# Performance work log

Hardware: AMD Instinct MI355X
Metric: run time of the kernel (lower is better)

## Reference

```python
import jax, jax.numpy as jnp
import numpy as np

EMBED_DIM = 1024
NUM_HEADS = 16
HEAD_DIM = EMBED_DIM // NUM_HEADS
SCALE = HEAD_DIM ** -0.5


def setup_inputs() -> dict:
    key = jax.random.key(0)
    k_x, k_qkv, k_proj = jax.random.split(key, 3)
    x = jax.random.normal(k_x, (2, 2048, EMBED_DIM), dtype=jnp.float32)
    # nn.Linear weights: [out_features, in_features]
    w_qkv = jax.random.normal(k_qkv, (3 * EMBED_DIM, EMBED_DIM), dtype=jnp.float32) * (EMBED_DIM ** -0.5)
    w_proj = jax.random.normal(k_proj, (EMBED_DIM, EMBED_DIM), dtype=jnp.float32) * (EMBED_DIM ** -0.5)
    return {"x": x, "w_qkv": w_qkv, "w_proj": w_proj}


def reference(x, w_qkv, w_proj):
    B, N, C = x.shape
    # fused QKV projection: [B,N,3C]
    qkv = jnp.einsum('bnc,oc->bno', x, w_qkv)
    qkv = qkv.reshape(B, N, 3, NUM_HEADS, HEAD_DIM)
    q, k, v = jnp.moveaxis(qkv, 2, 0)  # each [B, N, H, D]
    q = q.transpose(0, 2, 1, 3)  # [B, H, N, D]
    k = k.transpose(0, 2, 1, 3)
    v = v.transpose(0, 2, 1, 3)
    # scaled dot-product attention (eval mode: dropout_p=0, non-causal)
    scores = jnp.einsum('bhqd,bhkd->bhqk', q, k) * SCALE
    attn = jax.nn.softmax(scores, axis=-1)
    out = jnp.einsum('bhqk,bhkd->bhqd', attn, v)  # [B, H, N, D]
    out = out.transpose(0, 2, 1, 3).reshape(B, N, C)
    return jnp.einsum('bnc,oc->bno', out, w_proj)
```

## Files before the change

### kernel.cpp

```cpp
#include <hip/hip_runtime.h>
#include <hip/hip_bf16.h>

typedef __bf16 bf16;
typedef __bf16 bf16x8 __attribute__((ext_vector_type(8)));
typedef __bf16 bf16x4 __attribute__((ext_vector_type(4)));
typedef float f32x4 __attribute__((ext_vector_type(4)));

#define MFMA16(a, b, c) __builtin_amdgcn_mfma_f32_16x16x32_bf16(a, b, c, 0, 0, 0)

__global__ void cvt_kernel(const float* __restrict__ in, bf16* __restrict__ out, int n4) {
    int i = blockIdx.x * blockDim.x + threadIdx.x;
    if (i < n4) {
        float4 f = ((const float4*)in)[i];
        bf16x4 o;
        o[0] = (bf16)f.x; o[1] = (bf16)f.y; o[2] = (bf16)f.z; o[3] = (bf16)f.w;
        ((bf16x4*)out)[i] = o;
    }
}

__global__ __launch_bounds__(256, 2) void gemm_qkv(
    const bf16* __restrict__ A, const bf16* __restrict__ Bm,
    bf16* __restrict__ qo, bf16* __restrict__ ko, bf16* __restrict__ vo)
{
    const int K = 1024;
    __shared__ bf16 As[128][40];
    __shared__ bf16 Bs[128][40];
    const int tid = threadIdx.x;
    const int wave = tid >> 6, lane = tid & 63;
    const int lrow = lane & 15, quad = lane >> 4;
    const int wm = (wave >> 1) * 64, wn = (wave & 1) * 64;
    const int si = tid >> 2, sk = (tid & 3) * 8;

    const bf16* Ap = A + (long)(blockIdx.x * 128 + si) * K + sk;
    const bf16* Bp = Bm + (long)(blockIdx.y * 128 + si) * K + sk;

    f32x4 acc[4][4] = {};

    for (int k0 = 0; k0 < K; k0 += 32) {
        bf16x8 a0 = *(const bf16x8*)(Ap + k0);
        bf16x8 a1 = *(const bf16x8*)(Ap + (long)64 * K + k0);
        bf16x8 b0 = *(const bf16x8*)(Bp + k0);
        bf16x8 b1 = *(const bf16x8*)(Bp + (long)64 * K + k0);
        __syncthreads();
        *(bf16x8*)&As[si][sk]      = a0;
        *(bf16x8*)&As[si + 64][sk] = a1;
        *(bf16x8*)&Bs[si][sk]      = b0;
        *(bf16x8*)&Bs[si + 64][sk] = b1;
        __syncthreads();
        bf16x8 af[4], bfr[4];
#pragma unroll
        for (int i = 0; i < 4; i++) af[i] = *(const bf16x8*)&As[wm + i * 16 + lrow][quad * 8];
#pragma unroll
        for (int j = 0; j < 4; j++) bfr[j] = *(const bf16x8*)&Bs[wn + j * 16 + lrow][quad * 8];
#pragma unroll
        for (int i = 0; i < 4; i++)
#pragma unroll
            for (int j = 0; j < 4; j++)
                acc[i][j] = MFMA16(af[i], bfr[j], acc[i][j]);
    }

    const int gm0 = blockIdx.x * 128 + wm;
    const int go0 = blockIdx.y * 128 + wn;

    if (blockIdx.y < 16) {
        const bool isQ = blockIdx.y < 8;
        bf16* dst = isQ ? qo : ko;
        const float sc = isQ ? 0.125f : 1.0f;
#pragma unroll
        for (int i = 0; i < 4; i++) {
#pragma unroll
            for (int r = 0; r < 4; r++) {
                int gm = gm0 + i * 16 + quad * 4 + r;
                int b = gm >> 11, n = gm & 2047;
#pragma unroll
                for (int j = 0; j < 4; j++) {
                    int o = go0 + j * 16 + lrow;
                    int rem = o & 1023;
                    int h = rem >> 6, d = rem & 63;
                    long idx = (((long)(b * 16 + h)) * 2048 + n) * 64 + d;
                    dst[idx] = (bf16)(acc[i][j][r] * sc);
                }
            }
        }
    } else {
#pragma unroll
        for (int i = 0; i < 4; i++) {
            int gmb = gm0 + i * 16 + quad * 4;
            int b = gmb >> 11, nb = gmb & 2047;
#pragma unroll
            for (int j = 0; j < 4; j++) {
                int o = go0 + j * 16 + lrow;
                int rem = o & 1023;
                int h = rem >> 6, d = rem & 63;
                bf16x4 pk;
#pragma unroll
                for (int r = 0; r < 4; r++) pk[r] = (bf16)acc[i][j][r];
                *(bf16x4*)&vo[(((long)(b * 16 + h)) * 64 + d) * 2048 + nb] = pk;
            }
        }
    }
}

__global__ __launch_bounds__(256, 2) void attn_kernel(
    const bf16* __restrict__ q, const bf16* __restrict__ k,
    const bf16* __restrict__ vt, bf16* __restrict__ o)
{
    __shared__ bf16 Ks[64][72];
    __shared__ bf16 Vts[64][72];
    __shared__ bf16 QP[128][72];

    const int tid = threadIdx.x, wave = tid >> 6, lane = tid & 63;
    const int lrow = lane & 15, quad = lane >> 4;
    const int bh = blockIdx.x, qt = blockIdx.y;
    const bf16* Qp = q + ((long)bh * 2048 + qt * 128) * 64;
    const bf16* Kp = k + (long)bh * 2048 * 64;
    const bf16* Vp = vt + (long)bh * 64 * 2048;

    {
        int r0 = tid >> 3, g = (tid & 7) * 8;
#pragma unroll
        for (int p = 0; p < 4; p++)
            *(bf16x8*)&QP[r0 + p * 32][g] = *(const bf16x8*)&Qp[(r0 + p * 32) * 64 + g];
    }
    __syncthreads();
    bf16x8 qf[2][2];
#pragma unroll
    for (int t = 0; t < 2; t++)
#pragma unroll
        for (int ks = 0; ks < 2; ks++)
            qf[t][ks] = *(const bf16x8*)&QP[wave * 32 + t * 16 + lrow][ks * 32 + quad * 8];

    bf16(*Ps)[72] = (bf16(*)[72])QP + wave * 32;

    float mst[2] = {-1e30f, -1e30f}, lst[2] = {0.0f, 0.0f};
    f32x4 oacc[2][4] = {};

    for (int kv = 0; kv < 32; kv++) {
        const int r0 = tid >> 3, g = (tid & 7) * 8;
        const bf16* Kt = Kp + kv * 64 * 64;
        bf16x8 k0v = *(const bf16x8*)&Kt[r0 * 64 + g];
        bf16x8 k1v = *(const bf16x8*)&Kt[(r0 + 32) * 64 + g];
        bf16x8 v0v = *(const bf16x8*)&Vp[(long)r0 * 2048 + kv * 64 + g];
        bf16x8 v1v = *(const bf16x8*)&Vp[(long)(r0 + 32) * 2048 + kv * 64 + g];
        __syncthreads();
        *(bf16x8*)&Ks[r0][g]       = k0v;
        *(bf16x8*)&Ks[r0 + 32][g]  = k1v;
        *(bf16x8*)&Vts[r0][g]      = v0v;
        *(bf16x8*)&Vts[r0 + 32][g] = v1v;
        __syncthreads();

        f32x4 sacc[2][4] = {};
#pragma unroll
        for (int ks = 0; ks < 2; ks++) {
            bf16x8 kf[4];
#pragma unroll
            for (int n = 0; n < 4; n++) kf[n] = *(const bf16x8*)&Ks[n * 16 + lrow][ks * 32 + quad * 8];
#pragma unroll
            for (int t = 0; t < 2; t++)
#pragma unroll
                for (int n = 0; n < 4; n++)
                    sacc[t][n] = MFMA16(kf[n], qf[t][ks], sacc[t][n]);
        }

#pragma unroll
        for (int t = 0; t < 2; t++) {
            float mx = -1e30f;
#pragma unroll
            for (int n = 0; n < 4; n++)
#pragma unroll
                for (int r = 0; r < 4; r++) mx = fmaxf(mx, sacc[t][n][r]);
            mx = fmaxf(mx, __shfl_xor(mx, 16, 64));
            mx = fmaxf(mx, __shfl_xor(mx, 32, 64));
            float mnew = fmaxf(mst[t], mx);
            float alpha = __expf(mst[t] - mnew);
            mst[t] = mnew;
            float rsum = 0.0f;
#pragma unroll
            for (int n = 0; n < 4; n++) {
                bf16x4 pk;
#pragma unroll
                for (int r = 0; r < 4; r++) {
                    float p = __expf(sacc[t][n][r] - mnew);
                    rsum += p;
                    pk[r] = (bf16)p;
                }
                *(bf16x4*)&Ps[t * 16 + lrow][n * 16 + quad * 4] = pk;
            }
            rsum += __shfl_xor(rsum, 16, 64);
            rsum += __shfl_xor(rsum, 32, 64);
            lst[t] = lst[t] * alpha + rsum;
            float a0 = __shfl(alpha, quad * 4 + 0, 64);
            float a1 = __shfl(alpha, quad * 4 + 1, 64);
            float a2 = __shfl(alpha, quad * 4 + 2, 64);
            float a3 = __shfl(alpha, quad * 4 + 3, 64);
#pragma unroll
            for (int jd = 0; jd < 4; jd++) {
                oacc[t][jd][0] *= a0; oacc[t][jd][1] *= a1;
                oacc[t][jd][2] *= a2; oacc[t][jd][3] *= a3;
            }
        }

#pragma unroll
        for (int c = 0; c < 2; c++) {
            bf16x8 vf[4];
#pragma unroll
            for (int jd = 0; jd < 4; jd++)
                vf[jd] = *(const bf16x8*)&Vts[jd * 16 + lrow][c * 32 + quad * 8];
#pragma unroll
            for (int t = 0; t < 2; t++) {
                bf16x8 pf = *(const bf16x8*)&Ps[t * 16 + lrow][c * 32 + quad * 8];
#pragma unroll
                for (int jd = 0; jd < 4; jd++)
                    oacc[t][jd] = MFMA16(pf, vf[jd], oacc[t][jd]);
            }
        }
    }

    const int b = bh >> 4, h = bh & 15;
#pragma unroll
    for (int t = 0; t < 2; t++) {
        float linv = 1.0f / lst[t];
#pragma unroll
        for (int r = 0; r < 4; r++) {
            float lr = __shfl(linv, quad * 4 + r, 64);
            int n = qt * 128 + wave * 32 + t * 16 + quad * 4 + r;
#pragma unroll
            for (int jd = 0; jd < 4; jd++)
                o[((long)(b * 2048 + n)) * 1024 + h * 64 + jd * 16 + lrow] = (bf16)(oacc[t][jd][r] * lr);
        }
    }
}

__global__ __launch_bounds__(256, 2) void gemm_proj(
    const bf16* __restrict__ A, const bf16* __restrict__ Bm, float* __restrict__ out)
{
    const int K = 1024;
    __shared__ bf16 As[128][40];
    __shared__ bf16 Bs[128][40];
    const int tid = threadIdx.x;
    const int wave = tid >> 6, lane = tid & 63;
    const int lrow = lane & 15, quad = lane >> 4;
    const int wm = (wave >> 1) * 64, wn = (wave & 1) * 64;
    const int si = tid >> 2, sk = (tid & 3) * 8;

    const bf16* Ap = A + (long)(blockIdx.x * 128 + si) * K + sk;
    const bf16* Bp = Bm + (long)(blockIdx.y * 128 + si) * K + sk;

    f32x4 acc[4][4] = {};

    for (int k0 = 0; k0 < K; k0 += 32) {
        bf16x8 a0 = *(const bf16x8*)(Ap + k0);
        bf16x8 a1 = *(const bf16x8*)(Ap + (long)64 * K + k0);
        bf16x8 b0 = *(const bf16x8*)(Bp + k0);
        bf16x8 b1 = *(const bf16x8*)(Bp + (long)64 * K + k0);
        __syncthreads();
        *(bf16x8*)&As[si][sk]      = a0;
        *(bf16x8*)&As[si + 64][sk] = a1;
        *(bf16x8*)&Bs[si][sk]      = b0;
        *(bf16x8*)&Bs[si + 64][sk] = b1;
        __syncthreads();
        bf16x8 af[4], bfr[4];
#pragma unroll
        for (int i = 0; i < 4; i++) af[i] = *(const bf16x8*)&As[wm + i * 16 + lrow][quad * 8];
#pragma unroll
        for (int j = 0; j < 4; j++) bfr[j] = *(const bf16x8*)&Bs[wn + j * 16 + lrow][quad * 8];
#pragma unroll
        for (int i = 0; i < 4; i++)
#pragma unroll
            for (int j = 0; j < 4; j++)
                acc[i][j] = MFMA16(af[i], bfr[j], acc[i][j]);
    }

    const int gm0 = blockIdx.x * 128 + wm;
    const int go0 = blockIdx.y * 128 + wn;
#pragma unroll
    for (int i = 0; i < 4; i++)
#pragma unroll
        for (int r = 0; r < 4; r++) {
            int gm = gm0 + i * 16 + quad * 4 + r;
#pragma unroll
            for (int j = 0; j < 4; j++) {
                int o = go0 + j * 16 + lrow;
                out[(long)gm * 1024 + o] = acc[i][j][r];
            }
        }
}

extern "C" void kernel_launch(void* const* d_in, const int* in_sizes, int n_in,
                              void* d_out, int out_size, void* d_ws, size_t ws_size,
                              hipStream_t stream) {
    const float* x      = (const float*)d_in[0];
    const float* w_qkv  = (const float*)d_in[1];
    const float* w_proj = (const float*)d_in[2];
    float* out = (float*)d_out;

    bf16* ws = (bf16*)d_ws;
    bf16* xb     = ws;
    bf16* wqkvb  = xb + 4096 * 1024;
    bf16* wprojb = wqkvb + 3072 * 1024;
    bf16* qb     = wprojb + 1024 * 1024;
    bf16* kb     = qb + 2 * 16 * 2048 * 64;
    bf16* vb     = kb + 2 * 16 * 2048 * 64;
    bf16* ob     = vb + 2 * 16 * 2048 * 64;

    cvt_kernel<<<(4096 * 1024 / 4 + 255) / 256, 256, 0, stream>>>(x, xb, 4096 * 1024 / 4);
    cvt_kernel<<<(3072 * 1024 / 4 + 255) / 256, 256, 0, stream>>>(w_qkv, wqkvb, 3072 * 1024 / 4);
    cvt_kernel<<<(1024 * 1024 / 4 + 255) / 256, 256, 0, stream>>>(w_proj, wprojb, 1024 * 1024 / 4);

    gemm_qkv<<<dim3(32, 24), 256, 0, stream>>>(xb, wqkvb, qb, kb, vb);
    attn_kernel<<<dim3(32, 16), 256, 0, stream>>>(qb, kb, vb, ob);
    gemm_proj<<<dim3(32, 8), 256, 0, stream>>>(ob, wprojb, out);
}
```

Baseline: 205.3 us.

## Use direct global-to-LDS loads in GEMMs, register-direct K/V in attention

Both GEMMs now stage tiles with global_load_lds (direct global-to-LDS DMA) into unpadded 32-wide tiles, so the register round-trip disappears. The cost is more LDS bank conflicts on the fragment reads. The attention kernel drops shared-memory staging of Q, K and V: each wave loads its fragments straight from global memory into registers, prefetches the next K tile, and keeps only a per-wave P buffer, which removes the block-wide barriers. Attention grid indexing is flattened so heads vary fastest, and the projection GEMM uses 128x64 tiles to launch twice as many blocks. The trade-off is redundant global/L2 traffic for K/V across waves and uncoalesced strided V loads.

```diff
diff --git a/kernel.cpp b/kernel.cpp
--- a/kernel.cpp
+++ b/kernel.cpp
@@ -7,6 +7,12 @@
 typedef float f32x4 __attribute__((ext_vector_type(4)));
 
 #define MFMA16(a, b, c) __builtin_amdgcn_mfma_f32_16x16x32_bf16(a, b, c, 0, 0, 0)
+
+__device__ __forceinline__ void gll(const bf16* g, bf16* l) {
+    __builtin_amdgcn_global_load_lds(
+        (const __attribute__((address_space(1))) unsigned int*)g,
+        (__attribute__((address_space(3))) unsigned int*)l, 16, 0, 0);
+}
 
 __global__ void cvt_kernel(const float* __restrict__ in, bf16* __restrict__ out, int n4) {
     int i = blockIdx.x * blockDim.x + threadIdx.x;
@@ -22,36 +28,31 @@
     const bf16* __restrict__ A, const bf16* __restrict__ Bm,
     bf16* __restrict__ qo, bf16* __restrict__ ko, bf16* __restrict__ vo)
 {
-    const int K = 1024;
-    __shared__ bf16 As[128][40];
-    __shared__ bf16 Bs[128][40];
+    __shared__ bf16 As[128 * 32];
+    __shared__ bf16 Bs[128 * 32];
     const int tid = threadIdx.x;
     const int wave = tid >> 6, lane = tid & 63;
     const int lrow = lane & 15, quad = lane >> 4;
     const int wm = (wave >> 1) * 64, wn = (wave & 1) * 64;
-    const int si = tid >> 2, sk = (tid & 3) * 8;
-
-    const bf16* Ap = A + (long)(blockIdx.x * 128 + si) * K + sk;
-    const bf16* Bp = Bm + (long)(blockIdx.y * 128 + si) * K + sk;
+    const int row = tid >> 2, kcol = (tid & 3) * 8;
+
+    const bf16* Ap = A + (long)(blockIdx.x * 128 + row) * 1024 + kcol;
+    const bf16* Bp = Bm + (long)(blockIdx.y * 128 + row) * 1024 + kcol;
 
     f32x4 acc[4][4] = {};
 
-    for (int k0 = 0; k0 < K; k0 += 32) {
-        bf16x8 a0 = *(const bf16x8*)(Ap + k0);
-        bf16x8 a1 = *(const bf16x8*)(Ap + (long)64 * K + k0);
-        bf16x8 b0 = *(const bf16x8*)(Bp + k0);
-        bf16x8 b1 = *(const bf16x8*)(Bp + (long)64 * K + k0);
+    for (int k0 = 0; k0 < 1024; k0 += 32) {
         __syncthreads();
-        *(bf16x8*)&As[si][sk]      = a0;
-        *(bf16x8*)&As[si + 64][sk] = a1;
-        *(bf16x8*)&Bs[si][sk]      = b0;
-        *(bf16x8*)&Bs[si + 64][sk] = b1;
+        gll(Ap + k0,              As + tid * 8);
+        gll(Ap + 64 * 1024 + k0,  As + 2048 + tid * 8);
+        gll(Bp + k0,              Bs + tid * 8);
+        gll(Bp + 64 * 1024 + k0,  Bs + 2048 + tid * 8);
         __syncthreads();
         bf16x8 af[4], bfr[4];
 #pragma unroll
-        for (int i = 0; i < 4; i++) af[i] = *(const bf16x8*)&As[wm + i * 16 + lrow][quad * 8];
-#pragma unroll
-        for (int j = 0; j < 4; j++) bfr[j] = *(const bf16x8*)&Bs[wn + j * 16 + lrow][quad * 8];
+        for (int i = 0; i < 4; i++) af[i] = *(const bf16x8*)&As[(wm + i * 16 + lrow) * 32 + quad * 8];
+#pragma unroll
+        for (int j = 0; j < 4; j++) bfr[j] = *(const bf16x8*)&Bs[(wn + j * 16 + lrow) * 32 + quad * 8];
 #pragma unroll
         for (int i = 0; i < 4; i++)
 #pragma unroll
@@ -105,61 +106,58 @@
     const bf16* __restrict__ q, const bf16* __restrict__ k,
     const bf16* __restrict__ vt, bf16* __restrict__ o)
 {
-    __shared__ bf16 Ks[64][72];
-    __shared__ bf16 Vts[64][72];
-    __shared__ bf16 QP[128][72];
+    __shared__ bf16 Ps[4][32][72];
 
     const int tid = threadIdx.x, wave = tid >> 6, lane = tid & 63;
     const int lrow = lane & 15, quad = lane >> 4;
-    const int bh = blockIdx.x, qt = blockIdx.y;
-    const bf16* Qp = q + ((long)bh * 2048 + qt * 128) * 64;
+    const int bidx = blockIdx.x;
+    const int bh = bidx & 31, qt = bidx >> 5;
+    const bf16* Qp = q + ((long)bh * 2048 + qt * 128 + wave * 32) * 64;
     const bf16* Kp = k + (long)bh * 2048 * 64;
     const bf16* Vp = vt + (long)bh * 64 * 2048;
 
-    {
-        int r0 = tid >> 3, g = (tid & 7) * 8;
-#pragma unroll
-        for (int p = 0; p < 4; p++)
-            *(bf16x8*)&QP[r0 + p * 32][g] = *(const bf16x8*)&Qp[(r0 + p * 32) * 64 + g];
-    }
-    __syncthreads();
     bf16x8 qf[2][2];
 #pragma unroll
     for (int t = 0; t < 2; t++)
 #pragma unroll
         for (int ks = 0; ks < 2; ks++)
-            qf[t][ks] = *(const bf16x8*)&QP[wave * 32 + t * 16 + lrow][ks * 32 + quad * 8];
-
-    bf16(*Ps)[72] = (bf16(*)[72])QP + wave * 32;
+            qf[t][ks] = *(const bf16x8*)&Qp[(t * 16 + lrow) * 64 + ks * 32 + quad * 8];
 
     float mst[2] = {-1e30f, -1e30f}, lst[2] = {0.0f, 0.0f};
     f32x4 oacc[2][4] = {};
 
+    bf16x8 kf[2][4];
+#pragma unroll
+    for (int ks = 0; ks < 2; ks++)
+#pragma unroll
+        for (int n = 0; n < 4; n++)
+            kf[ks][n] = *(const bf16x8*)&Kp[(n * 16 + lrow) * 64 + ks * 32 + quad * 8];
+
     for (int kv = 0; kv < 32; kv++) {
-        const int r0 = tid >> 3, g = (tid & 7) * 8;
-        const bf16* Kt = Kp + kv * 64 * 64;
-        bf16x8 k0v = *(const bf16x8*)&Kt[r0 * 64 + g];
-        bf16x8 k1v = *(const bf16x8*)&Kt[(r0 + 32) * 64 + g];
-        bf16x8 v0v = *(const bf16x8*)&Vp[(long)r0 * 2048 + kv * 64 + g];
-        bf16x8 v1v = *(const bf16x8*)&Vp[(long)(r0 + 32) * 2048 + kv * 64 + g];
-        __syncthreads();
-        *(bf16x8*)&Ks[r0][g]       = k0v;
-        *(bf16x8*)&Ks[r0 + 32][g]  = k1v;
-        *(bf16x8*)&Vts[r0][g]      = v0v;
-        *(bf16x8*)&Vts[r0 + 32][g] = v1v;
-        __syncthreads();
+        bf16x8 vf[2][4];
+#pragma unroll
+        for (int c = 0; c < 2; c++)
+#pragma unroll
+            for (int jd = 0; jd < 4; jd++)
+                vf[c][jd] = *(const bf16x8*)&Vp[(long)(jd * 16 + lrow) * 2048 + kv * 64 + c * 32 + quad * 8];
 
         f32x4 sacc[2][4] = {};
 #pragma unroll
-        for (int ks = 0; ks < 2; ks++) {
-            bf16x8 kf[4];
-#pragma unroll
-            for (int n = 0; n < 4; n++) kf[n] = *(const bf16x8*)&Ks[n * 16 + lrow][ks * 32 + quad * 8];
+        for (int ks = 0; ks < 2; ks++)
 #pragma unroll
             for (int t = 0; t < 2; t++)
 #pragma unroll
                 for (int n = 0; n < 4; n++)
-                    sacc[t][n] = MFMA16(kf[n], qf[t][ks], sacc[t][n]);
+                    sacc[t][n] = MFMA16(kf[ks][n], qf[t][ks], sacc[t][n]);
+
+        {
+            int kn = (kv + 1) & 31;
+            const bf16* Kt = Kp + kn * 64 * 64;
+#pragma unroll
+            for (int ks = 0; ks < 2; ks++)
+#pragma unroll
+                for (int n = 0; n < 4; n++)
+                    kf[ks][n] = *(const bf16x8*)&Kt[(n * 16 + lrow) * 64 + ks * 32 + quad * 8];
         }
 
 #pragma unroll
@@ -184,7 +182,7 @@
                     rsum += p;
                     pk[r] = (bf16)p;
                 }
-                *(bf16x4*)&Ps[t * 16 + lrow][n * 16 + quad * 4] = pk;
+                *(bf16x4*)&Ps[wave][t * 16 + lrow][n * 16 + quad * 4] = pk;
             }
             rsum += __shfl_xor(rsum, 16, 64);
             rsum += __shfl_xor(rsum, 32, 64);
@@ -201,19 +199,14 @@
         }
 
 #pragma unroll
-        for (int c = 0; c < 2; c++) {
-            bf16x8 vf[4];
-#pragma unroll
-            for (int jd = 0; jd < 4; jd++)
-                vf[jd] = *(const bf16x8*)&Vts[jd * 16 + lrow][c * 32 + quad * 8];
+        for (int c = 0; c < 2; c++)
 #pragma unroll
             for (int t = 0; t < 2; t++) {
-                bf16x8 pf = *(const bf16x8*)&Ps[t * 16 + lrow][c * 32 + quad * 8];
+                bf16x8 pf = *(const bf16x8*)&Ps[wave][t * 16 + lrow][c * 32 + quad * 8];
 #pragma unroll
                 for (int jd = 0; jd < 4; jd++)
-                    oacc[t][jd] = MFMA16(pf, vf[jd], oacc[t][jd]);
-            }
-        }
+                    oacc[t][jd] = MFMA16(pf, vf[c][jd], oacc[t][jd]);
+            }
     }
 
     const int b = bh >> 4, h = bh & 15;
@@ -234,52 +227,46 @@
 __global__ __launch_bounds__(256, 2) void gemm_proj(
     const bf16* __restrict__ A, const bf16* __restrict__ Bm, float* __restrict__ out)
 {
-    const int K = 1024;
-    __shared__ bf16 As[128][40];
-    __shared__ bf16 Bs[128][40];
+    __shared__ bf16 As[128 * 32];
+    __shared__ bf16 Bs[64 * 32];
     const int tid = threadIdx.x;
     const int wave = tid >> 6, lane = tid & 63;
     const int lrow = lane & 15, quad = lane >> 4;
-    const int wm = (wave >> 1) * 64, wn = (wave & 1) * 64;
-    const int si = tid >> 2, sk = (tid & 3) * 8;
-
-    const bf16* Ap = A + (long)(blockIdx.x * 128 + si) * K + sk;
-    const bf16* Bp = Bm + (long)(blockIdx.y * 128 + si) * K + sk;
-
-    f32x4 acc[4][4] = {};
-
-    for (int k0 = 0; k0 < K; k0 += 32) {
-        bf16x8 a0 = *(const bf16x8*)(Ap + k0);
-        bf16x8 a1 = *(const bf16x8*)(Ap + (long)64 * K + k0);
-        bf16x8 b0 = *(const bf16x8*)(Bp + k0);
-        bf16x8 b1 = *(const bf16x8*)(Bp + (long)64 * K + k0);
+    const int wm = (wave >> 1) * 64, wn = (wave & 1) * 32;
+    const int row = tid >> 2, kcol = (tid & 3) * 8;
+
+    const bf16* Ap = A + (long)(blockIdx.x * 128 + row) * 1024 + kcol;
+    const bf16* Bp = Bm + (long)(blockIdx.y * 64 + row) * 1024 + kcol;
+
+    f32x4 acc[4][2] = {};
+
+    for (int k0 = 0; k0 < 1024; k0 += 32) {
         __syncthreads();
-        *(bf16x8*)&As[si][sk]      = a0;
-        *(bf16x8*)&As[si + 64][sk] = a1;
-        *(bf16x8*)&Bs[si][sk]      = b0;
-        *(bf16x8*)&Bs[si + 64][sk] = b1;
+        gll(Ap + k0,             As + tid * 8);
+        gll(Ap + 64 * 1024 + k0, As + 2048 + tid * 8);
+        gll(Bp + k0,             Bs + tid * 8);
         __syncthreads();
-        bf16x8 af[4], bfr[4];
-#pragma unroll
-        for (int i = 0; i < 4; i++) af[i] = *(const bf16x8*)&As[wm + i * 16 + lrow][quad * 8];
-#pragma unroll
-        for (int j = 0; j < 4; j++) bfr[j] = *(const bf16x8*)&Bs[wn + j * 16 + lrow][quad * 8];
+        bf16x8 af[4], bfr[2];
+#pragma unroll
+        for (int i = 0; i < 4; i++) af[i] = *(const bf16x8*)&As[(wm + i * 16 + lrow) * 32 + quad * 8];
+#pragma unroll
+        for (int j = 0; j < 2; j++) bfr[j] = *(const bf16x8*)&Bs[(wn + j * 16 + lrow) * 32 + quad * 8];
 #pragma unroll
         for (int i = 0; i < 4; i++)
 #pragma unroll
-            for (int j = 0; j < 4; j++)
+            for (int j = 0; j < 2; j++)
                 acc[i][j] = MFMA16(af[i], bfr[j], acc[i][j]);
     }
 
     const int gm0 = blockIdx.x * 128 + wm;
-    const int go0 = blockIdx.y * 128 + wn;
+    const int go0 = blockIdx.y * 64 + wn;
 #pragma unroll
     for (int i = 0; i < 4; i++)
 #pragma unroll
         for (int r = 0; r < 4; r++) {
             int gm = gm0 + i * 16 + quad * 4 + r;
 #pragma unroll
-            for (int j = 0; j < 4; j++) {
+            for (int j = 0; j < 2; j++) {
                 int o = go0 + j * 16 + lrow;
                 out[(long)gm * 1024 + o] = acc[i][j][r];
             }
@@ -308,6 +295,6 @@
     cvt_kernel<<<(1024 * 1024 / 4 + 255) / 256, 256, 0, stream>>>(w_proj, wprojb, 1024 * 1024 / 4);
 
     gemm_qkv<<<dim3(32, 24), 256, 0, stream>>>(xb, wqkvb, qb, kb, vb);
-    attn_kernel<<<dim3(32, 16), 256, 0, stream>>>(qb, kb, vb, ob);
-    gemm_proj<<<dim3(32, 8), 256, 0, stream>>>(ob, wprojb, out);
-}
+    attn_kernel<<<512, 256, 0, stream>>>(qb, kb, vb, ob);
+    gemm_proj<<<dim3(32, 16), 256, 0, stream>>>(ob, wprojb, out);
+}
```

After: 250.8 us. 1.22x slower.
